# Kernel optimization log

Measured on AMD Instinct MI355X. Metric: run time of the kernel, lower is better.

## Reference

```python
import jax, jax.numpy as jnp
import numpy as np

B, LQ, LK = 2, 2048, 77
DIM, XDIM = 320, 768
H, HD = 8, 40  # heads, head_dim; DIM == H*HD
FF = 4 * DIM  # GEGLU inner dim


def _ln(x, g, b, eps=1e-5):
    m = x.mean(-1, keepdims=True)
    v = ((x - m) ** 2).mean(-1, keepdims=True)
    return (x - m) * jax.lax.rsqrt(v + eps) * g + b


def _split_heads(x):  # [B,L,DIM] -> [B,H,L,HD]
    return x.reshape(x.shape[0], x.shape[1], H, HD).transpose(0, 2, 1, 3)


def _merge_heads(x):  # [B,H,L,HD] -> [B,L,DIM]
    return x.transpose(0, 2, 1, 3).reshape(x.shape[0], x.shape[2], H * HD)


def setup_inputs() -> dict:
    key = jax.random.key(0)
    ks = jax.random.split(key, 24)
    s = 0.02
    r = lambda i, shp: s * jax.random.normal(ks[i], shp, jnp.float32)
    return {
        "hidden_states": jax.random.normal(ks[0], (B, LQ, DIM), jnp.float32),
        "encoder_hidden_states": jax.random.normal(ks[1], (B, LK, XDIM), jnp.float32),
        # norm1 + self-attn (attn1)
        "ln1_g": jnp.ones((DIM,), jnp.float32), "ln1_b": jnp.zeros((DIM,), jnp.float32),
        "wq1": r(2, (DIM, DIM)), "wk1": r(3, (DIM, DIM)), "wv1": r(4, (DIM, DIM)),
        "wo1": r(5, (DIM, DIM)), "bo1": jnp.zeros((DIM,), jnp.float32),
        # norm2 + Hadamard cross-attn (attn2)
        "ln2_g": jnp.ones((DIM,), jnp.float32), "ln2_b": jnp.zeros((DIM,), jnp.float32),
        "wq2": r(6, (DIM, DIM)), "wk2": r(7, (XDIM, DIM)), "wvh": r(8, (DIM, DIM)),
        "wo2": r(9, (DIM, DIM)), "bo2": jnp.zeros((DIM,), jnp.float32),
        # norm3 + GEGLU feed-forward
        "ln3_g": jnp.ones((DIM,), jnp.float32), "ln3_b": jnp.zeros((DIM,), jnp.float32),
        "wff1": r(10, (DIM, 2 * FF)), "bff1": jnp.zeros((2 * FF,), jnp.float32),
        "wff2": r(11, (FF, DIM)), "bff2": jnp.zeros((DIM,), jnp.float32),
    }


def reference(hidden_states, encoder_hidden_states, ln1_g, ln1_b, wq1, wk1, wv1,
              wo1, bo1, ln2_g, ln2_b, wq2, wk2, wvh, wo2, bo2, ln3_g, ln3_b,
              wff1, bff1, wff2, bff2):
    scale = 1.0 / jnp.sqrt(jnp.asarray(HD, hidden_states.dtype))

    # ---- self-attention (SDPA semantics) ----
    h = _ln(hidden_states, ln1_g, ln1_b)
    q = _split_heads(h @ wq1)
    k = _split_heads(h @ wk1)
    v = _split_heads(h @ wv1)
    scores = jnp.einsum('bhqd,bhkd->bhqk', q, k) * scale
    w = jax.nn.softmax(scores, axis=-1)
    attn = jnp.einsum('bhqk,bhkd->bhqd', w, v)
    attn = _merge_heads(attn) @ wo1 + bo1
    hidden_states = hidden_states + attn

    # ---- Hadamard cross-attention: value comes from hidden_states (len Lq) ----
    h = _ln(hidden_states, ln2_g, ln2_b)
    q = _split_heads(h @ wq2)                     # [B,H,Lq,HD]
    k = _split_heads(encoder_hidden_states @ wk2) # [B,H,Lk,HD]
    vH = _split_heads(h @ wvh)                    # [B,H,Lq,HD]
    scores = jnp.einsum('bhqd,bhkd->bhqk', q, k) * scale
    w = jax.nn.softmax(scores, axis=-1)           # [B,H,Lq,Lk]
    # (w[...,None] * vH[...,None,:]).sum(-2) == vH * w.sum(-1, keepdims) (v indep of k)
    cross = vH * jnp.sum(w, axis=-1, keepdims=True)
    cross = _merge_heads(cross) @ wo2 + bo2
    hidden_states = hidden_states + cross

    # ---- GEGLU feed-forward ----
    h = _ln(hidden_states, ln3_g, ln3_b)
    proj = h @ wff1 + bff1
    x, gate = jnp.split(proj, 2, axis=-1)
    ff = (x * jax.nn.gelu(gate, approximate=False)) @ wff2 + bff2
    return hidden_states + ff
```

## Files before the change

### kernel.cpp

```cpp
#include <hip/hip_runtime.h>
#include <math.h>

#define DIM   320
#define HD    40
#define NH    8
#define LQ    2048
#define BATCH 2
#define MROWS 4096
#define FFD   1280
#define FF2   2560

#define KSPLIT 8
#define KCHUNK (LQ/KSPLIT)
#define KT     32
#define NT     (KCHUNK/KT)
#define NQROWS (BATCH*NH*LQ)

#define LSCALE (0.15811388300841897f * 1.4426950408889634f)

typedef unsigned short ushort_t;
typedef unsigned int u32;
using bf16x8 = __attribute__((ext_vector_type(8))) short;
using f32x4  = __attribute__((ext_vector_type(4))) float;

static __device__ inline ushort_t f2bf(float f) {
  union { float f; unsigned u; } x{f};
  unsigned r = x.u + 0x7FFFu + ((x.u >> 16) & 1u);
  return (ushort_t)(r >> 16);
}
static __device__ inline float bf2f(ushort_t h) {
  union { unsigned u; float f; } x; x.u = ((unsigned)h) << 16; return x.f;
}

__global__ __launch_bounds__(256) void ln_kernel(
    const float* __restrict__ X, const float* __restrict__ g,
    const float* __restrict__ bta, ushort_t* __restrict__ Y)
{
  int row  = blockIdx.x * 4 + (threadIdx.x >> 6);
  int lane = threadIdx.x & 63;
  const float* x = X + (size_t)row * DIM;
  float v[5];
  float s = 0.f;
#pragma unroll
  for (int i = 0; i < 5; ++i) { v[i] = x[lane + 64*i]; s += v[i]; }
#pragma unroll
  for (int off = 32; off >= 1; off >>= 1) s += __shfl_xor(s, off, 64);
  float mean = s * (1.0f/DIM);
  float sq = 0.f;
#pragma unroll
  for (int i = 0; i < 5; ++i) { float d = v[i] - mean; sq += d*d; }
#pragma unroll
  for (int off = 32; off >= 1; off >>= 1) sq += __shfl_xor(sq, off, 64);
  float rstd = rsqrtf(sq*(1.0f/DIM) + 1e-5f);
  ushort_t* y = Y + (size_t)row * DIM;
#pragma unroll
  for (int i = 0; i < 5; ++i) {
    int c = lane + 64*i;
    y[c] = f2bf((v[i]-mean)*rstd*g[c] + bta[c]);
  }
}

#define OFF_WQKVT 0
#define OFF_WO1T  (960*320)
#define OFF_WO2T  (OFF_WO1T + 320*320)
#define OFF_WFF1T (OFF_WO2T + 320*320)
#define OFF_WFF2T (OFF_WFF1T + 320*2560)
#define OFF_WVHB  (OFF_WFF2T + 1280*320)
#define WBF_TOTAL (OFF_WVHB + 320*320)

__global__ __launch_bounds__(256) void convw_kernel(
    const float* __restrict__ wq1, const float* __restrict__ wk1,
    const float* __restrict__ wv1, const float* __restrict__ wo1,
    const float* __restrict__ wo2, const float* __restrict__ wff1,
    const float* __restrict__ wff2, const float* __restrict__ wvh,
    ushort_t* __restrict__ dst, ushort_t* __restrict__ Kimg)
{
  int e = blockIdx.y;
  if (e == 8) {
    int f = blockIdx.x*256 + threadIdx.x;
    if (f < 98304) {
      int g3 = f/3, cidx = f - 3*g3;
      int rr = g3 & 31, tile = (g3 >> 5) & 63, bh = g3 >> 11;
      uint4 z = {0,0,0,0};
      *(uint4*)(Kimg + ((size_t)(bh*64 + tile))*2048 + rr*64
                + (((5+cidx) ^ (rr&7)) << 3)) = z;
    }
    return;
  }
  const float* src; int K, N; size_t doff; int tr = 1; float scale = 1.f;
  switch (e) {
    case 0: src=wq1;  K=320;  N=320;  doff=OFF_WQKVT; scale=LSCALE; break;
    case 1: src=wk1;  K=320;  N=320;  doff=OFF_WQKVT + 320*320;  break;
    case 2: src=wv1;  K=320;  N=320;  doff=OFF_WQKVT + 2*320*320;break;
    case 3: src=wo1;  K=320;  N=320;  doff=OFF_WO1T;             break;
    case 4: src=wo2;  K=320;  N=320;  doff=OFF_WO2T;             break;
    case 5: src=wff1; K=320;  N=2560; doff=OFF_WFF1T;            break;
    case 6: src=wff2; K=1280; N=320;  doff=OFF_WFF2T;            break;
    default: src=wvh; K=320;  N=320;  doff=OFF_WVHB; tr=0;       break;
  }
  int ntN = N/32;
  int nt_total = (K/32)*ntN;
  int t = blockIdx.x;
  if (t >= nt_total) return;
  int kt = t / ntN, nt = t - kt*ntN;
  __shared__ float tile[32][33];
  int tx = threadIdx.x & 31, ty = threadIdx.x >> 5;
  ushort_t* d = dst + doff;
#pragma unroll
  for (int i = 0; i < 4; ++i) {
    int r = ty + 8*i;
    tile[r][tx] = src[(size_t)(kt*32+r)*N + nt*32+tx] * scale;
  }
  __syncthreads();
  if (tr) {
#pragma unroll
    for (int i = 0; i < 4; ++i) {
      int r = ty + 8*i;
      d[(size_t)(nt*32+r)*K + kt*32+tx] = f2bf(tile[tx][r]);
    }
  } else {
#pragma unroll
    for (int i = 0; i < 4; ++i) {
      int r = ty + 8*i;
      d[(size_t)(kt*32+r)*N + nt*32+tx] = f2bf(tile[r][tx]);
    }
  }
}

#define AST 72
__global__ __launch_bounds__(256) void mgemm(
    const ushort_t* __restrict__ A, int lda,
    const ushort_t* __restrict__ Bt, int ldb,
    const float* __restrict__ bias,
    const float* __restrict__ R,
    float* __restrict__ Cf, ushort_t* __restrict__ Cb, int ldc,
    int K)
{
  __shared__ ushort_t As[64*AST];
  __shared__ ushort_t Bs[64*AST];
  int tid = threadIdx.x;
  int w = tid >> 6, lane = tid & 63, quad = lane >> 4, n16 = lane & 15;
  int wm = w >> 1, wn = w & 1;
  int bm = blockIdx.y * 64, bn = blockIdx.x * 64;
  int sr = tid >> 2, sc = (tid & 3) << 4;
  const ushort_t* Ag = A  + (size_t)(bm + sr)*lda + sc;
  const ushort_t* Bg = Bt + (size_t)(bn + sr)*ldb + sc;

  f32x4 acc00 = {0.f,0.f,0.f,0.f}, acc01 = acc00, acc10 = acc00, acc11 = acc00;

  float4 av0 = *(const float4*)(Ag);
  float4 av1 = *(const float4*)(Ag + 8);
  float4 bv0 = *(const float4*)(Bg);
  float4 bv1 = *(const float4*)(Bg + 8);
  for (int k0 = 0; k0 < K; k0 += 64) {
    __syncthreads();
    *(float4*)(As + sr*AST + sc)     = av0;
    *(float4*)(As + sr*AST + sc + 8) = av1;
    *(float4*)(Bs + sr*AST + sc)     = bv0;
    *(float4*)(Bs + sr*AST + sc + 8) = bv1;
    __syncthreads();
    if (k0 + 64 < K) {
      av0 = *(const float4*)(Ag + k0 + 64);
      av1 = *(const float4*)(Ag + k0 + 72);
      bv0 = *(const float4*)(Bg + k0 + 64);
      bv1 = *(const float4*)(Bg + k0 + 72);
    }
#pragma unroll
    for (int kk = 0; kk < 64; kk += 32) {
      bf16x8 fa0 = *(const bf16x8*)(As + (wm*32 +      n16)*AST + kk + quad*8);
      bf16x8 fa1 = *(const bf16x8*)(As + (wm*32 + 16 + n16)*AST + kk + quad*8);
      bf16x8 fb0 = *(const bf16x8*)(Bs + (wn*32 +      n16)*AST + kk + quad*8);
      bf16x8 fb1 = *(const bf16x8*)(Bs + (wn*32 + 16 + n16)*AST + kk + quad*8);
      acc00 = __builtin_amdgcn_mfma_f32_16x16x32_bf16(fa0, fb0, acc00, 0,0,0);
      acc01 = __builtin_amdgcn_mfma_f32_16x16x32_bf16(fa0, fb1, acc01, 0,0,0);
      acc10 = __builtin_amdgcn_mfma_f32_16x16x32_bf16(fa1, fb0, acc10, 0,0,0);
      acc11 = __builtin_amdgcn_mfma_f32_16x16x32_bf16(fa1, fb1, acc11, 0,0,0);
    }
  }

  f32x4 accs[2][2] = {{acc00, acc01},{acc10, acc11}};
#pragma unroll
  for (int s = 0; s < 2; ++s)
#pragma unroll
    for (int t = 0; t < 2; ++t) {
      int c = bn + wn*32 + t*16 + n16;
      float bb = bias ? bias[c] : 0.f;
#pragma unroll
      for (int i = 0; i < 4; ++i) {
        int r = bm + wm*32 + s*16 + quad*4 + i;
        float v = accs[s][t][i] + bb;
        if (R)  v += R[(size_t)r*ldc + c];
        if (Cf) Cf[(size_t)r*ldc + c] = v;
        if (Cb) Cb[(size_t)r*ldc + c] = f2bf(v);
      }
    }
}

#define AS_STRIDE 40
__global__ __launch_bounds__(256) void mgemm128_qkv(
    const ushort_t* __restrict__ A, const ushort_t* __restrict__ Bt,
    ushort_t* __restrict__ Qb, ushort_t* __restrict__ Kimg,
    ushort_t* __restrict__ Vimg)
{
  __shared__ ushort_t As[128*AS_STRIDE];
  __shared__ ushort_t Bs[64*AS_STRIDE];
  int tid = threadIdx.x;
  int w = tid >> 6, lane = tid & 63, quad = lane >> 4, n16 = lane & 15;
  int wm = w >> 1, wn = w & 1;
  int bm = blockIdx.y * 128, bn = blockIdx.x * 64;
  int ar = tid >> 1, ac = (tid & 1) << 4;
  int br = tid >> 2, bc = (tid & 3) << 3;
  const ushort_t* Ag = A  + (size_t)(bm + ar)*DIM + ac;
  const ushort_t* Bg = Bt + (size_t)(bn + br)*DIM + bc;

  f32x4 acc[4][2];
#pragma unroll
  for (int s = 0; s < 4; ++s)
#pragma unroll
    for (int t = 0; t < 2; ++t) acc[s][t] = f32x4{0.f,0.f,0.f,0.f};

  float4 av0 = *(const float4*)(Ag);
  float4 av1 = *(const float4*)(Ag + 8);
  float4 bv  = *(const float4*)(Bg);
  for (int k0 = 0; k0 < DIM; k0 += 32) {
    __syncthreads();
    *(float4*)(As + ar*AS_STRIDE + ac)     = av0;
    *(float4*)(As + ar*AS_STRIDE + ac + 8) = av1;
    *(float4*)(Bs + br*AS_STRIDE + bc)     = bv;
    __syncthreads();
    if (k0 + 32 < DIM) {
      av0 = *(const float4*)(Ag + k0 + 32);
      av1 = *(const float4*)(Ag + k0 + 40);
      bv  = *(const float4*)(Bg + k0 + 32);
    }
    bf16x8 fa[4], fb[2];
#pragma unroll
    for (int s = 0; s < 4; ++s)
      fa[s] = *(const bf16x8*)(As + (wm*64 + s*16 + n16)*AS_STRIDE + quad*8);
#pragma unroll
    for (int t = 0; t < 2; ++t)
      fb[t] = *(const bf16x8*)(Bs + (wn*32 + t*16 + n16)*AS_STRIDE + quad*8);
#pragma unroll
    for (int s = 0; s < 4; ++s)
#pragma unroll
      for (int t = 0; t < 2; ++t)
        acc[s][t] = __builtin_amdgcn_mfma_f32_16x16x32_bf16(fa[s], fb[t], acc[s][t], 0,0,0);
  }

  int b8 = (bm >> 11) << 3;
  if (bn < 320) {
#pragma unroll
    for (int s = 0; s < 4; ++s)
#pragma unroll
      for (int t = 0; t < 2; ++t) {
        int c = bn + wn*32 + t*16 + n16;
#pragma unroll
        for (int i = 0; i < 4; ++i) {
          int r = bm + wm*64 + s*16 + quad*4 + i;
          Qb[(size_t)r*320 + c] = f2bf(acc[s][t][i]);
        }
      }
  } else if (bn < 640) {
#pragma unroll
    for (int t = 0; t < 2; ++t) {
      int c = bn + wn*32 + t*16 + n16 - 320;
      int hK = c / 40, d = c - hK*40;
      ushort_t* kb = Kimg + ((size_t)(b8 + hK))*64*2048
                   + (((d >> 3) ^ 0) << 3) + (d & 7);
#pragma unroll
      for (int s = 0; s < 4; ++s)
#pragma unroll
        for (int i = 0; i < 4; ++i) {
          int r = bm + wm*64 + s*16 + quad*4 + i;
          int l = r & 2047, tl = l >> 5, rr = l & 31;
          Kimg[((size_t)((b8 + hK)*64 + tl))*2048 + rr*64
               + (((d >> 3) ^ (rr & 7)) << 3) + (d & 7)] = f2bf(acc[s][t][i]);
        }
      (void)kb;
    }
  } else {
#pragma unroll
    for (int t = 0; t < 2; ++t) {
      int c = bn + wn*32 + t*16 + n16 - 640;
      int hV = c / 40, d = c - hV*40;
#pragma unroll
      for (int s = 0; s < 4; ++s) {
        int l0 = (bm + wm*64 + s*16 + quad*4) & 2047;
        int tl = l0 >> 5, p0 = (l0 & 31) >> 1;
        ushort_t* vb = Vimg + ((size_t)((b8 + hV)*64 + tl))*1536 + d*32;
#pragma unroll
        for (int j = 0; j < 2; ++j) {
          int p = p0 + j;
          unsigned val = (unsigned)f2bf(acc[s][t][2*j])
                       | ((unsigned)f2bf(acc[s][t][2*j+1]) << 16);
          *(unsigned*)(vb + (((p >> 2) ^ (d & 3)) << 3) + ((p & 3) << 1)) = val;
        }
      }
    }
  }
}

__global__ __launch_bounds__(256) void ff1_geglu(
    const ushort_t* __restrict__ A, const ushort_t* __restrict__ Bt,
    const float* __restrict__ bias, ushort_t* __restrict__ Og)
{
  __shared__ ushort_t As[128*AS_STRIDE];
  __shared__ ushort_t Bxs[64*AS_STRIDE];
  __shared__ ushort_t Bgs[64*AS_STRIDE];
  int tid = threadIdx.x;
  int w = tid >> 6, lane = tid & 63, quad = lane >> 4, n16 = lane & 15;
  int wm = w >> 1, wn = w & 1;
  int bm = blockIdx.y * 128, bn = blockIdx.x * 64;
  int ar = tid >> 1, ac = (tid & 1) << 4;
  int br = tid >> 2, bc = (tid & 3) << 3;
  const ushort_t* Ag  = A  + (size_t)(bm + ar)*DIM + ac;
  const ushort_t* Bxg = Bt + (size_t)(bn + br)*DIM + bc;
  const ushort_t* Bgg = Bt + (size_t)(bn + FFD + br)*DIM + bc;

  f32x4 ax[4][2], ag[4][2];
#pragma unroll
  for (int s = 0; s < 4; ++s)
#pragma unroll
    for (int t = 0; t < 2; ++t) { ax[s][t] = f32x4{0.f,0.f,0.f,0.f}; ag[s][t] = ax[s][t]; }

  float4 av0 = *(const float4*)(Ag);
  float4 av1 = *(const float4*)(Ag + 8);
  float4 bxv = *(const float4*)(Bxg);
  float4 bgv = *(const float4*)(Bgg);
  for (int k0 = 0; k0 < DIM; k0 += 32) {
    __syncthreads();
    *(float4*)(As  + ar*AS_STRIDE + ac)     = av0;
    *(float4*)(As  + ar*AS_STRIDE + ac + 8) = av1;
    *(float4*)(Bxs + br*AS_STRIDE + bc)     = bxv;
    *(float4*)(Bgs + br*AS_STRIDE + bc)     = bgv;
    __syncthreads();
    if (k0 + 32 < DIM) {
      av0 = *(const float4*)(Ag  + k0 + 32);
      av1 = *(const float4*)(Ag  + k0 + 40);
      bxv = *(const float4*)(Bxg + k0 + 32);
      bgv = *(const float4*)(Bgg + k0 + 32);
    }
    bf16x8 fa[4], fx[2], fg[2];
#pragma unroll
    for (int s = 0; s < 4; ++s)
      fa[s] = *(const bf16x8*)(As + (wm*64 + s*16 + n16)*AS_STRIDE + quad*8);
#pragma unroll
    for (int t = 0; t < 2; ++t) {
      fx[t] = *(const bf16x8*)(Bxs + (wn*32 + t*16 + n16)*AS_STRIDE + quad*8);
      fg[t] = *(const bf16x8*)(Bgs + (wn*32 + t*16 + n16)*AS_STRIDE + quad*8);
    }
#pragma unroll
    for (int s = 0; s < 4; ++s)
#pragma unroll
      for (int t = 0; t < 2; ++t) {
        ax[s][t] = __builtin_amdgcn_mfma_f32_16x16x32_bf16(fa[s], fx[t], ax[s][t], 0,0,0);
        ag[s][t] = __builtin_amdgcn_mfma_f32_16x16x32_bf16(fa[s], fg[t], ag[s][t], 0,0,0);
      }
  }

  const float kk = 0.7071067811865476f;
#pragma unroll
  for (int s = 0; s < 4; ++s)
#pragma unroll
    for (int t = 0; t < 2; ++t) {
      int c = bn + wn*32 + t*16 + n16;
      float bx = bias[c], bg = bias[c + FFD];
#pragma unroll
      for (int i = 0; i < 4; ++i) {
        int r = bm + wm*64 + s*16 + quad*4 + i;
        float xx = ax[s][t][i] + bx;
        float gg = ag[s][t][i] + bg;
        Og[(size_t)r*FFD + c] = f2bf(xx * 0.5f * gg * (1.f + erff(gg * kk)));
      }
    }
}

#define TILE_K_SH 2048
#define TILE_V_SH 1536
#define TILE_SH   (TILE_K_SH + TILE_V_SH)

__global__ __launch_bounds__(256, 2) void attn_mfma(
    const ushort_t* __restrict__ Qb, const ushort_t* __restrict__ Kimg,
    const ushort_t* __restrict__ Vimg,
    float* __restrict__ Pl, ushort_t* __restrict__ Pacc)
{
  __shared__ ushort_t lds[2*TILE_SH];
  int tid  = threadIdx.x;
  int w    = tid >> 6;
  int lane = tid & 63;
  int quad = lane >> 4;
  int n16  = lane & 15;

  int blk  = blockIdx.x;
  int bh   = (blk & 7) | (((blk >> 3) & 1) << 3);
  int rest = blk >> 4;
  int qt   = rest & 15;
  int ks   = rest >> 4;
  int b = bh >> 3, h = bh & 7;

  const ushort_t* qrowa = Qb + (size_t)(b*LQ + qt*128 + w*32 + n16)*320 + h*HD;
  const ushort_t* qrowb = qrowa + 16*320;
  bf16x8 qf0a = *(const bf16x8*)(qrowa + quad*8);
  bf16x8 qf1a = *(const bf16x8*)(qrowa + 32);
  bf16x8 qf0b = *(const bf16x8*)(qrowb + quad*8);
  bf16x8 qf1b = *(const bf16x8*)(qrowb + 32);

  const ushort_t* Ktb = Kimg + ((size_t)bh*64 + ks*NT)*TILE_K_SH;
  const ushort_t* Vtb = Vimg + ((size_t)bh*64 + ks*NT)*TILE_V_SH;

  int swk0 = (quad ^ (n16 & 7)) << 3;
  int swk1 = ((quad + 4) ^ (n16 & 7)) << 3;
  int kof0 = n16*64 + swk0;
  int kof1 = n16*64 + swk1;
  int kof2 = (16+n16)*64 + swk0;
  int kof3 = (16+n16)*64 + swk1;
  int swv  = (quad ^ (n16 & 3)) << 3;
  int vof0 = n16*32 + swv;
  int vof1 = (16+n16)*32 + swv;
  int vof2 = (32+n16)*32 + swv;

  f32x4 o0a = {0.f,0.f,0.f,0.f}, o1a = o0a, o2a = o0a;
  f32x4 o0b = o0a, o1b = o0a, o2b = o0a;
  f32x4 la0a = o0a, la1a = o0a, la0b = o0a, la1b = o0a;

#define CVTPK(D, LO, HI) \
  asm("v_cvt_pk_bf16_f32 %0, %1, %2" : "=v"(D) : "v"(LO), "v"(HI))
#define PSWAP32(X, Y) \
  asm("v_permlane32_swap_b32 %0, %1" : "+v"(X), "+v"(Y))
#define PSWAP16(X, Y) \
  asm("v_permlane16_swap_b32 %0, %1" : "+v"(X), "+v"(Y))

#define STAGE(BUF, T) { \
  const ushort_t* ks_ = Ktb + (size_t)(T)*TILE_K_SH + w*512 + lane*8; \
  ushort_t* kd_ = lds + (BUF)*TILE_SH + w*512; \
  __builtin_amdgcn_global_load_lds( \
      (const __attribute__((address_space(1))) u32*)ks_, \
      (__attribute__((address_space(3))) u32*)kd_, 16, 0, 0); \
  if (w < 3) { \
    const ushort_t* vs_ = Vtb + (size_t)(T)*TILE_V_SH + w*512 + lane*8; \
    ushort_t* vd_ = lds + (BUF)*TILE_SH + TILE_K_SH + w*512; \
    __builtin_amdgcn_global_load_lds( \
        (const __attribute__((address_space(1))) u32*)vs_, \
        (__attribute__((address_space(3))) u32*)vd_, 16, 0, 0); \
  } }

#define HALF(Q0F, Q1F, LA0, LA1, FRAG) \
  bf16x8 FRAG; { \
  f32x4 st0 = {-8.f,-8.f,-8.f,-8.f}; f32x4 st1 = st0; \
  st0 = __builtin_amdgcn_mfma_f32_16x16x32_bf16(K00, Q0F, st0, 0,0,0); \
  st1 = __builtin_amdgcn_mfma_f32_16x16x32_bf16(K10, Q0F, st1, 0,0,0); \
  st0 = __builtin_amdgcn_mfma_f32_16x16x32_bf16(K01, Q1F, st0, 0,0,0); \
  st1 = __builtin_amdgcn_mfma_f32_16x16x32_bf16(K11, Q1F, st1, 0,0,0); \
  f32x4 p0, p1; \
  _Pragma("unroll") \
  for (int r = 0; r < 4; ++r) { p0[r] = exp2f(st0[r]); p1[r] = exp2f(st1[r]); } \
  LA0 += p0; LA1 += p1; \
  unsigned d0, d1, d2, d3; \
  CVTPK(d0, p0[0], p0[1]); CVTPK(d1, p0[2], p0[3]); \
  CVTPK(d2, p1[0], p1[1]); CVTPK(d3, p1[2], p1[3]); \
  PSWAP32(d0, d2); PSWAP16(d0, d2); \
  PSWAP32(d1, d3); PSWAP16(d1, d3); \
  union { unsigned u[4]; bf16x8 v; } fr_; \
  fr_.u[0] = d0; fr_.u[1] = d1; fr_.u[2] = d2; fr_.u[3] = d3; \
  FRAG = fr_.v; }

  STAGE(0, 0);
  __syncthreads();
  for (int t = 0; t < NT; ++t) {
    int buf = t & 1;
    if (t + 1 < NT) STAGE(buf^1, t+1);
    const ushort_t* Kb_ = lds + buf*TILE_SH;
    const ushort_t* Vb_ = Kb_ + TILE_K_SH;
    bf16x8 K00 = *(const bf16x8*)(Kb_ + kof0);
    bf16x8 K01 = *(const bf16x8*)(Kb_ + kof1);
    bf16x8 K10 = *(const bf16x8*)(Kb_ + kof2);
    bf16x8 K11 = *(const bf16x8*)(Kb_ + kof3);
    bf16x8 V0  = *(const bf16x8*)(Vb_ + vof0);
    bf16x8 V1  = *(const bf16x8*)(Vb_ + vof1);
    bf16x8 V2  = *(const bf16x8*)(Vb_ + vof2);
    HALF(qf0a, qf1a, la0a, la1a, fragA)
    HALF(qf0b, qf1b, la0b, la1b, fragB)
    o0a = __builtin_amdgcn_mfma_f32_16x16x32_bf16(fragA, V0, o0a, 0,0,0);
    o0b = __builtin_amdgcn_mfma_f32_16x16x32_bf16(fragB, V0, o0b, 0,0,0);
    o1a = __builtin_amdgcn_mfma_f32_16x16x32_bf16(fragA, V1, o1a, 0,0,0);
    o1b = __builtin_amdgcn_mfma_f32_16x16x32_bf16(fragB, V1, o1b, 0,0,0);
    o2a = __builtin_amdgcn_mfma_f32_16x16x32_bf16(fragA, V2, o2a, 0,0,0);
    o2b = __builtin_amdgcn_mfma_f32_16x16x32_bf16(fragB, V2, o2b, 0,0,0);
    __syncthreads();
  }
#undef STAGE
#undef HALF
#undef CVTPK
#undef PSWAP32
#undef PSWAP16

  float sA = la0a[0]+la0a[1]+la0a[2]+la0a[3] + la1a[0]+la1a[1]+la1a[2]+la1a[3];
  float sB = la0b[0]+la0b[1]+la0b[2]+la0b[3] + la1b[0]+la1b[1]+la1b[2]+la1b[3];
  sA += __shfl_xor(sA, 16, 64); sA += __shfl_xor(sA, 32, 64);
  sB += __shfl_xor(sB, 16, 64); sB += __shfl_xor(sB, 32, 64);

  int grow = bh*LQ + qt*128 + w*32;
  size_t base = (size_t)ks*NQROWS;
  if (lane < 16) {
    Pl[base + grow + n16]      = sA;
    Pl[base + grow + 16 + n16] = sB;
  }

  int gqa = grow + quad*4;
#pragma unroll
  for (int r = 0; r < 4; ++r) {
    size_t gq = base + gqa + r;
    ushort_t* pw = Pacc + gq*40;
    pw[n16]      = f2bf(o0a[r]);
    pw[16 + n16] = f2bf(o1a[r]);
    if (n16 < 8) pw[32 + n16] = f2bf(o2a[r]);
    size_t gq2 = gq + 16;
    ushort_t* pw2 = Pacc + gq2*40;
    pw2[n16]      = f2bf(o0b[r]);
    pw2[16 + n16] = f2bf(o1b[r]);
    if (n16 < 8) pw2[32 + n16] = f2bf(o2b[r]);
  }
}

__global__ __launch_bounds__(256) void attn_merge(
    const float* __restrict__ Pl, const ushort_t* __restrict__ Pacc,
    ushort_t* __restrict__ O)
{
  int idx = blockIdx.x*256 + threadIdx.x;
  int bh = idx >> 11, qi = idx & (LQ-1);
  int b = bh >> 3, h = bh & 7;
  float L = 0.f;
#pragma unroll
  for (int k = 0; k < KSPLIT; ++k) L += Pl[(size_t)k*NQROWS + idx];
  float inv = 1.0f / L;
  ushort_t* orow = O + (size_t)(b*LQ + qi)*DIM + h*HD;
#pragma unroll
  for (int u = 0; u < 5; ++u) {
    float acc[8] = {0,0,0,0,0,0,0,0};
#pragma unroll
    for (int k = 0; k < KSPLIT; ++k) {
      const ushort_t* pr = Pacc + ((size_t)k*NQROWS + idx)*40 + u*8;
      ushort_t vbuf[8];
      *(uint4*)vbuf = *(const uint4*)pr;
#pragma unroll
      for (int j = 0; j < 8; ++j) acc[j] += bf2f(vbuf[j]);
    }
    ushort_t ob[8];
#pragma unroll
    for (int j = 0; j < 8; ++j) ob[j] = f2bf(acc[j]*inv);
    *(uint4*)(orow + u*8) = *(uint4*)ob;
  }
}

extern "C" void kernel_launch(void* const* d_in, const int* in_sizes, int n_in,
                              void* d_out, int out_size, void* d_ws, size_t ws_size,
                              hipStream_t stream) {
  const float* hidden = (const float*)d_in[0];
  const float* ln1_g = (const float*)d_in[2];
  const float* ln1_b = (const float*)d_in[3];
  const float* wq1   = (const float*)d_in[4];
  const float* wk1   = (const float*)d_in[5];
  const float* wv1   = (const float*)d_in[6];
  const float* wo1   = (const float*)d_in[7];
  const float* bo1   = (const float*)d_in[8];
  const float* ln2_g = (const float*)d_in[9];
  const float* ln2_b = (const float*)d_in[10];
  const float* wvh   = (const float*)d_in[13];
  const float* wo2   = (const float*)d_in[14];
  const float* bo2   = (const float*)d_in[15];
  const float* ln3_g = (const float*)d_in[16];
  const float* ln3_b = (const float*)d_in[17];
  const float* wff1  = (const float*)d_in[18];
  const float* bff1  = (const float*)d_in[19];
  const float* wff2  = (const float*)d_in[20];
  const float* bff2  = (const float*)d_in[21];
  float* out = (float*)d_out;

  ushort_t* wsu = (ushort_t*)d_ws;
  ushort_t* wbf   = wsu;
  ushort_t* lnb   = wbf + WBF_TOTAL;
  ushort_t* Qb    = lnb + (size_t)MROWS*DIM;
  ushort_t* attnb = Qb + (size_t)MROWS*DIM;
  ushort_t* gegb  = attnb + (size_t)MROWS*DIM;
  ushort_t* wct   = gegb + (size_t)MROWS*FFD;
  ushort_t* vtb   = wct + 320*320;
  ushort_t* kpb   = vtb + (size_t)16*64*1536;
  ushort_t* Pacc  = kpb + (size_t)16*64*2048;
  float* fws = (float*)((((uintptr_t)(Pacc + (size_t)KSPLIT*NQROWS*40)) + 255) & ~(uintptr_t)255);
  float* h1   = fws;
  float* h2   = h1 + (size_t)MROWS*DIM;
  float* Pl   = h2 + (size_t)MROWS*DIM;

  dim3 t256(256);
  dim3 gconv(1024, 9);
  dim3 gqkv(15, 32);
  dim3 g320(5, 64);
  dim3 gwc(5, 5);
  dim3 gffg(20, 32);
  dim3 gattn(16*16*KSPLIT);

  convw_kernel<<<gconv, t256, 0, stream>>>(wq1, wk1, wv1, wo1, wo2, wff1, wff2,
                                           wvh, wbf, kpb);
  mgemm<<<gwc, t256, 0, stream>>>(wbf + OFF_WO2T, DIM, wbf + OFF_WVHB, DIM,
                                  nullptr, nullptr, nullptr, wct, DIM, DIM);

  ln_kernel<<<MROWS/4, t256, 0, stream>>>(hidden, ln1_g, ln1_b, lnb);
  mgemm128_qkv<<<gqkv, t256, 0, stream>>>(lnb, wbf + OFF_WQKVT, Qb, kpb, vtb);
  attn_mfma<<<gattn, t256, 0, stream>>>(Qb, kpb, vtb, Pl, Pacc);
  attn_merge<<<NQROWS/256, t256, 0, stream>>>(Pl, Pacc, attnb);
  mgemm<<<g320, t256, 0, stream>>>(attnb, DIM, wbf + OFF_WO1T, DIM, bo1, hidden,
                                   h1, nullptr, DIM, DIM);

  ln_kernel<<<MROWS/4, t256, 0, stream>>>(h1, ln2_g, ln2_b, lnb);
  mgemm<<<g320, t256, 0, stream>>>(lnb, DIM, wct, DIM, bo2, h1,
                                   h2, nullptr, DIM, DIM);

  ln_kernel<<<MROWS/4, t256, 0, stream>>>(h2, ln3_g, ln3_b, lnb);
  ff1_geglu<<<gffg, t256, 0, stream>>>(lnb, wbf + OFF_WFF1T, bff1, gegb);
  mgemm<<<g320, t256, 0, stream>>>(gegb, FFD, wbf + OFF_WFF2T, FFD, bff2, h2,
                                   out, nullptr, DIM, FFD);
}
```

Measured before the change: 225.8 us.

## Stage two K/V tiles per barrier in attention loop to halve syncs

The attention kernel's K/V pipeline now loads two 32-key tiles per stage into a doubled LDS buffer (four tile slots) and computes both before a single __syncthreads. This halves the number of barriers and gives the async global-to-LDS loads more time to land. It doubles LDS use per block, roughly 14 KB to 28 KB, which could limit occupancy, and it assumes NT is even. It also removes an unused pointer computation in the QKV GEMM epilogue.

```diff
diff --git a/kernel.cpp b/kernel.cpp
--- a/kernel.cpp
+++ b/kernel.cpp
@@ -265,8 +265,6 @@
     for (int t = 0; t < 2; ++t) {
       int c = bn + wn*32 + t*16 + n16 - 320;
       int hK = c / 40, d = c - hK*40;
-      ushort_t* kb = Kimg + ((size_t)(b8 + hK))*64*2048
-                   + (((d >> 3) ^ 0) << 3) + (d & 7);
 #pragma unroll
       for (int s = 0; s < 4; ++s)
 #pragma unroll
@@ -276,7 +274,6 @@
           Kimg[((size_t)((b8 + hK)*64 + tl))*2048 + rr*64
                + (((d >> 3) ^ (rr & 7)) << 3) + (d & 7)] = f2bf(acc[s][t][i]);
         }
-      (void)kb;
     }
   } else {
 #pragma unroll
@@ -384,7 +381,7 @@
     const ushort_t* __restrict__ Vimg,
     float* __restrict__ Pl, ushort_t* __restrict__ Pacc)
 {
-  __shared__ ushort_t lds[2*TILE_SH];
+  __shared__ ushort_t lds[4*TILE_SH];
   int tid  = threadIdx.x;
   int w    = tid >> 6;
   int lane = tid & 63;
@@ -430,15 +427,15 @@
 #define PSWAP16(X, Y) \
   asm("v_permlane16_swap_b32 %0, %1" : "+v"(X), "+v"(Y))
 
-#define STAGE(BUF, T) { \
+#define STAGE(SLOT, T) { \
   const ushort_t* ks_ = Ktb + (size_t)(T)*TILE_K_SH + w*512 + lane*8; \
-  ushort_t* kd_ = lds + (BUF)*TILE_SH + w*512; \
+  ushort_t* kd_ = lds + (SLOT)*TILE_SH + w*512; \
   __builtin_amdgcn_global_load_lds( \
       (const __attribute__((address_space(1))) u32*)ks_, \
       (__attribute__((address_space(3))) u32*)kd_, 16, 0, 0); \
   if (w < 3) { \
     const ushort_t* vs_ = Vtb + (size_t)(T)*TILE_V_SH + w*512 + lane*8; \
-    ushort_t* vd_ = lds + (BUF)*TILE_SH + TILE_K_SH + w*512; \
+    ushort_t* vd_ = lds + (SLOT)*TILE_SH + TILE_K_SH + w*512; \
     __builtin_amdgcn_global_load_lds( \
         (const __attribute__((address_space(1))) u32*)vs_, \
         (__attribute__((address_space(3))) u32*)vd_, 16, 0, 0); \
@@ -464,31 +461,39 @@
   fr_.u[0] = d0; fr_.u[1] = d1; fr_.u[2] = d2; fr_.u[3] = d3; \
   FRAG = fr_.v; }
 
-  STAGE(0, 0);
+#define CTILE(SLOT) { \
+  const ushort_t* Kb_ = lds + (SLOT)*TILE_SH; \
+  const ushort_t* Vb_ = Kb_ + TILE_K_SH; \
+  bf16x8 K00 = *(const bf16x8*)(Kb_ + kof0); \
+  bf16x8 K01 = *(const bf16x8*)(Kb_ + kof1); \
+  bf16x8 K10 = *(const bf16x8*)(Kb_ + kof2); \
+  bf16x8 K11 = *(const bf16x8*)(Kb_ + kof3); \
+  bf16x8 V0  = *(const bf16x8*)(Vb_ + vof0); \
+  bf16x8 V1  = *(const bf16x8*)(Vb_ + vof1); \
+  bf16x8 V2  = *(const bf16x8*)(Vb_ + vof2); \
+  HALF(qf0a, qf1a, la0a, la1a, fragA) \
+  HALF(qf0b, qf1b, la0b, la1b, fragB) \
+  o0a = __builtin_amdgcn_mfma_f32_16x16x32_bf16(fragA, V0, o0a, 0,0,0); \
+  o0b = __builtin_amdgcn_mfma_f32_16x16x32_bf16(fragB, V0, o0b, 0,0,0); \
+  o1a = __builtin_amdgcn_mfma_f32_16x16x32_bf16(fragA, V1, o1a, 0,0,0); \
+  o1b = __builtin_amdgcn_mfma_f32_16x16x32_bf16(fragB, V1, o1b, 0,0,0); \
+  o2a = __builtin_amdgcn_mfma_f32_16x16x32_bf16(fragA, V2, o2a, 0,0,0); \
+  o2b = __builtin_amdgcn_mfma_f32_16x16x32_bf16(fragB, V2, o2b, 0,0,0); }
+
+  STAGE(0, 0); STAGE(1, 1);
   __syncthreads();
-  for (int t = 0; t < NT; ++t) {
-    int buf = t & 1;
-    if (t + 1 < NT) STAGE(buf^1, t+1);
-    const ushort_t* Kb_ = lds + buf*TILE_SH;
-    const ushort_t* Vb_ = Kb_ + TILE_K_SH;
-    bf16x8 K00 = *(const bf16x8*)(Kb_ + kof0);
-    bf16x8 K01 = *(const bf16x8*)(Kb_ + kof1);
-    bf16x8 K10 = *(const bf16x8*)(Kb_ + kof2);
-    bf16x8 K11 = *(const bf16x8*)(Kb_ + kof3);
-    bf16x8 V0  = *(const bf16x8*)(Vb_ + vof0);
-    bf16x8 V1  = *(const bf16x8*)(Vb_ + vof1);
-    bf16x8 V2  = *(const bf16x8*)(Vb_ + vof2);
-    HALF(qf0a, qf1a, la0a, la1a, fragA)
-    HALF(qf0b, qf1b, la0b, la1b, fragB)
-    o0a = __builtin_amdgcn_mfma_f32_16x16x32_bf16(fragA, V0, o0a, 0,0,0);
-    o0b = __builtin_amdgcn_mfma_f32_16x16x32_bf16(fragB, V0, o0b, 0,0,0);
-    o1a = __builtin_amdgcn_mfma_f32_16x16x32_bf16(fragA, V1, o1a, 0,0,0);
-    o1b = __builtin_amdgcn_mfma_f32_16x16x32_bf16(fragB, V1, o1b, 0,0,0);
-    o2a = __builtin_amdgcn_mfma_f32_16x16x32_bf16(fragA, V2, o2a, 0,0,0);
-    o2b = __builtin_amdgcn_mfma_f32_16x16x32_bf16(fragB, V2, o2b, 0,0,0);
+  for (int s = 0; s < NT/2; ++s) {
+    int sb = s & 1;
+    if (s + 1 < NT/2) {
+      STAGE((sb^1)*2,     2*s + 2);
+      STAGE((sb^1)*2 + 1, 2*s + 3);
+    }
+    CTILE(sb*2);
+    CTILE(sb*2 + 1);
     __syncthreads();
   }
 #undef STAGE
+#undef CTILE
 #undef HALF
 #undef CVTPK
 #undef PSWAP32
```

Result: no change. 224.5 us (-0.6%).
